# Kernel optimization log

Measured on AMD Instinct MI355X. Metric: run time of the kernel, lower is better.

The kernel has to match this reference:

```python
import jax, jax.numpy as jnp
import numpy as np

B, H, S, D = 4, 16, 2048, 64

def setup_inputs() -> dict:
    key = jax.random.key(0)
    kq, kk, kv = jax.random.split(key, 3)
    return {
        "input_query": jax.random.normal(kq, (B, H, S, D), dtype=jnp.float32),
        "input_key": jax.random.normal(kk, (B, H, S, D), dtype=jnp.float32),
        "input_value": jax.random.normal(kv, (B, H, S, D), dtype=jnp.float32),
    }

def reference(input_query, input_key, input_value):
    # Unscaled, unmasked attention: softmax(Q K^T) V
    scores = jnp.einsum("bhsd,bhtd->bhst", input_query, input_key)  # [B,H,S,S]
    probs = jax.nn.softmax(scores, axis=-1)
    return jnp.einsum("bhst,bhtd->bhsd", probs, input_value)  # [B,H,S,D]
```

## Files before the change

kernel.cpp:

```cpp
#include <hip/hip_runtime.h>
#include <hip/hip_bf16.h>
#include <stdint.h>

#define SEQ 2048
#define DIM 64
#define NH  64
#define KT  32
#define NT  (SEQ / KT)
#define RAW_BYTES  16384
#define FRAG_BYTES 12288
#define KF_BYTES   8192

typedef __attribute__((ext_vector_type(8)))  short    bf16x8;
typedef __attribute__((ext_vector_type(8)))  _Float16 f16x8;
typedef __attribute__((ext_vector_type(16))) float    f32x16;
typedef unsigned int u32;

#if __has_builtin(__builtin_amdgcn_exp2f)
#define EXP2(x) __builtin_amdgcn_exp2f(x)
#else
#define EXP2(x) exp2f(x)
#endif

__device__ __forceinline__ int phi(int s) {
    int h = (s >> 2) & 1, b = s >> 3, i = s & 3;
    return 8 * h + 4 * b + i + (b >= 2 ? 8 : 0);
}
__device__ __forceinline__ short f2bf(float f) {
    union { float f; u32 u; } v; v.f = f;
    u32 r = v.u + 0x7fffu + ((v.u >> 16) & 1u);
    return (short)(r >> 16);
}

__device__ __forceinline__ void stage_tile(const float* gK, const float* gV,
                                           char* raw, int wave, int lane) {
    #pragma unroll
    for (int i = 0; i < 2; ++i) {
        const int P  = wave * 128 + i * 64 + lane;
        const int sk = (P & ~15) | ((P & 15) ^ ((P >> 4) & 7));
        char* dK = raw + (size_t)(wave * 128 + i * 64) * 16;
        char* dV = raw + 8192 + (size_t)(wave * 128 + i * 64) * 16;
        __builtin_amdgcn_global_load_lds(
            (const __attribute__((address_space(1))) u32*)((const char*)gK + (size_t)sk * 16),
            (__attribute__((address_space(3))) u32*)dK, 16, 0, 0);
        __builtin_amdgcn_global_load_lds(
            (const __attribute__((address_space(1))) u32*)((const char*)gV + (size_t)P * 16),
            (__attribute__((address_space(3))) u32*)dV, 16, 0, 0);
    }
}

__device__ __forceinline__ void convert_tile(const char* raw, char* frag, int t) {
    const int lane = t & 63, col = lane & 31, h = lane >> 5;
    {
        const int c = t >> 6;
        const int r = phi(col);
        const int kk = 4 * c + 2 * h;
        const float4* rk = (const float4*)raw;
        float4 a = rk[r * 16 + ((kk    ) ^ (r & 7))];
        float4 b = rk[r * 16 + ((kk + 1) ^ (r & 7))];
        float x[8] = {a.x, a.y, a.z, a.w, b.x, b.y, b.z, b.w};
        f16x8 hi, lo;
        #pragma unroll
        for (int j = 0; j < 8; ++j) {
            _Float16 xh = (_Float16)x[j];
            hi[j] = xh;
            lo[j] = (_Float16)(x[j] - (float)xh);
        }
        *(f16x8*)(frag + (c * 2 + 0) * 1024 + lane * 16) = hi;
        *(f16x8*)(frag + (c * 2 + 1) * 1024 + lane * 16) = lo;
    }
    {
        const int f = t >> 7, c = (t >> 6) & 1;
        const float* rv = (const float*)(raw + 8192);
        bf16x8 v;
        #pragma unroll
        for (int j = 0; j < 8; ++j) {
            int key = phi(16 * c + 8 * h + j);
            v[j] = f2bf(rv[key * 64 + f * 32 + col]);
        }
        *(bf16x8*)(frag + KF_BYTES + (f * 2 + c) * 1024 + lane * 16) = v;
    }
}

__global__ __launch_bounds__(256, 2) void attn_fused(
    const float* __restrict__ Q, const float* __restrict__ K,
    const float* __restrict__ V, float* __restrict__ O)
{
    __shared__ __align__(16) char raw[2][RAW_BYTES];
    __shared__ __align__(16) char frag[2][FRAG_BYTES];

    const int tid  = threadIdx.x;
    const int wave = tid >> 6, lane = tid & 63;
    const int h = lane >> 5, col = lane & 31;
    const int head = blockIdx.x >> 3;
    const int qb = (blockIdx.x & 7) * 256 + wave * 64;
    const size_t base = (size_t)head * SEQ * DIM;
    const float* Kh = K + base;
    const float* Vh = V + base;

    f16x8 qf[2][4];
    #pragma unroll
    for (int qt = 0; qt < 2; ++qt) {
        const float* qr = Q + base + (size_t)(qb + qt * 32 + col) * DIM;
        #pragma unroll
        for (int c = 0; c < 4; ++c)
            #pragma unroll
            for (int j = 0; j < 8; ++j)
                qf[qt][c][j] = (_Float16)(qr[c * 16 + 8 * h + j] * 1.44269504088896f);
    }

    f32x16 z16;
    #pragma unroll
    for (int r = 0; r < 16; ++r) z16[r] = 0.f;
    f32x16 of[2][2];
    of[0][0] = z16; of[0][1] = z16; of[1][0] = z16; of[1][1] = z16;
    float l_own[2] = {0.f, 0.f};

    stage_tile(Kh, Vh, raw[0], wave, lane);
    __syncthreads();
    convert_tile(raw[0], frag[0], tid);
    stage_tile(Kh + KT * DIM, Vh + KT * DIM, raw[1], wave, lane);

    for (int kt = 0; kt < NT; ++kt) {
        __syncthreads();
        if (kt < NT - 2)
            stage_tile(Kh + (size_t)(kt + 2) * KT * DIM,
                       Vh + (size_t)(kt + 2) * KT * DIM, raw[kt & 1], wave, lane);
        const char* cur = frag[kt & 1];

        f32x16 s[2]; s[0] = z16; s[1] = z16;
        #pragma unroll
        for (int c = 0; c < 4; ++c) {
            f16x8 kh = *(const f16x8*)(cur + (c * 2 + 0) * 1024 + lane * 16);
            f16x8 kl = *(const f16x8*)(cur + (c * 2 + 1) * 1024 + lane * 16);
            s[0] = __builtin_amdgcn_mfma_f32_32x32x16_f16(kh, qf[0][c], s[0], 0, 0, 0);
            s[0] = __builtin_amdgcn_mfma_f32_32x32x16_f16(kl, qf[0][c], s[0], 0, 0, 0);
            s[1] = __builtin_amdgcn_mfma_f32_32x32x16_f16(kh, qf[1][c], s[1], 0, 0, 0);
            s[1] = __builtin_amdgcn_mfma_f32_32x32x16_f16(kl, qf[1][c], s[1], 0, 0, 0);
        }

        bf16x8 pfrag[2][2];
        #pragma unroll
        for (int qt = 0; qt < 2; ++qt) {
            float p[16], ls = 0.f;
            #pragma unroll
            for (int r = 0; r < 16; ++r) { p[r] = EXP2(s[qt][r]); ls += p[r]; }
            l_own[qt] += ls;
            u32 pk[8], sw[8];
            #pragma unroll
            for (int m = 0; m < 8; ++m) {
                __hip_bfloat162 b2 = __float22bfloat162_rn(make_float2(p[2 * m], p[2 * m + 1]));
                __builtin_memcpy(&pk[m], &b2, 4);
            }
            #pragma unroll
            for (int m = 0; m < 8; ++m) sw[m] = __shfl_xor(pk[m], 32);
            #pragma unroll
            for (int c = 0; c < 2; ++c) {
                union { u32 w[4]; bf16x8 v; } fr;
                fr.w[0] = h ? sw[4 * c + 2] : pk[4 * c + 0];
                fr.w[1] = h ? sw[4 * c + 3] : pk[4 * c + 1];
                fr.w[2] = h ? pk[4 * c + 2] : sw[4 * c + 0];
                fr.w[3] = h ? pk[4 * c + 3] : sw[4 * c + 1];
                pfrag[qt][c] = fr.v;
            }
        }

        #pragma unroll
        for (int f = 0; f < 2; ++f)
            #pragma unroll
            for (int c = 0; c < 2; ++c) {
                bf16x8 vf = *(const bf16x8*)(cur + KF_BYTES + (f * 2 + c) * 1024 + lane * 16);
                of[0][f] = __builtin_amdgcn_mfma_f32_32x32x16_bf16(pfrag[0][c], vf, of[0][f], 0, 0, 0);
                of[1][f] = __builtin_amdgcn_mfma_f32_32x32x16_bf16(pfrag[1][c], vf, of[1][f], 0, 0, 0);
            }

        if (kt < NT - 1)
            convert_tile(raw[(kt + 1) & 1], frag[(kt + 1) & 1], tid);
    }

    float* op = O + base;
    #pragma unroll
    for (int qt = 0; qt < 2; ++qt) {
        float lall = l_own[qt] + __shfl_xor(l_own[qt], 32);
        float inv = 1.0f / lall;
        #pragma unroll
        for (int r = 0; r < 16; ++r) {
            int qrow = (r & 3) + 8 * (r >> 2) + 4 * h;
            float iq = __shfl(inv, qrow);
            op[(size_t)(qb + qt * 32 + qrow) * DIM + col]      = of[qt][0][r] * iq;
            op[(size_t)(qb + qt * 32 + qrow) * DIM + 32 + col] = of[qt][1][r] * iq;
        }
    }
}

extern "C" void kernel_launch(void* const* d_in, const int* in_sizes, int n_in,
                              void* d_out, int out_size, void* d_ws, size_t ws_size,
                              hipStream_t stream) {
    const float* Q = (const float*)d_in[0];
    const float* K = (const float*)d_in[1];
    const float* V = (const float*)d_in[2];
    float* Out = (float*)d_out;
    (void)d_ws; (void)ws_size;

    attn_fused<<<dim3(NH * (SEQ / 256)), dim3(256), 0, stream>>>(Q, K, V, Out);
}
```

Measured before the change: 238.5 us.

## Load K/V tiles directly into registers, drop raw LDS staging, raise occupancy

Replaces the global_load_lds staging into a raw LDS buffer with direct per-thread global loads into registers, issued one tile ahead and converted into the fragment buffer after compute. This removes 32KB of raw LDS per block, so launch bounds go from 2 to 3 blocks per SM. Block-to-head mapping is also remapped so that consecutive blocks cover different heads. The trade-offs are higher register pressure, a prefetch distance of one tile instead of two, and V loads that gather strided scalars.

```diff
diff --git a/kernel.cpp b/kernel.cpp
--- a/kernel.cpp
+++ b/kernel.cpp
@@ -7,7 +7,6 @@
 #define NH  64
 #define KT  32
 #define NT  (SEQ / KT)
-#define RAW_BYTES  16384
 #define FRAG_BYTES 12288
 #define KF_BYTES   8192
 
@@ -32,33 +31,39 @@
     return (short)(r >> 16);
 }
 
-__device__ __forceinline__ void stage_tile(const float* gK, const float* gV,
-                                           char* raw, int wave, int lane) {
+__global__ __launch_bounds__(256, 3) void attn_fused(
+    const float* __restrict__ Q, const float* __restrict__ K,
+    const float* __restrict__ V, float* __restrict__ O)
+{
+    __shared__ __align__(16) char frag[2][FRAG_BYTES];
+
+    const int tid  = threadIdx.x;
+    const int wave = tid >> 6, lane = tid & 63;
+    const int h = lane >> 5, col = lane & 31;
+
+    const int bid  = blockIdx.x;
+    const int head = (bid & 7) * 8 + ((bid >> 3) & 7);
+    const int qb   = (bid >> 6) * 256 + wave * 64;
+    const size_t base = (size_t)head * SEQ * DIM;
+
+    const float* kbase = K + base + (size_t)phi(col) * DIM + wave * 16 + 8 * h;
+    const int fv = tid >> 7, cv = (tid >> 6) & 1;
+    int vrow[8];
     #pragma unroll
-    for (int i = 0; i < 2; ++i) {
-        const int P  = wave * 128 + i * 64 + lane;
-        const int sk = (P & ~15) | ((P & 15) ^ ((P >> 4) & 7));
-        char* dK = raw + (size_t)(wave * 128 + i * 64) * 16;
-        char* dV = raw + 8192 + (size_t)(wave * 128 + i * 64) * 16;
-        __builtin_amdgcn_global_load_lds(
-            (const __attribute__((address_space(1))) u32*)((const char*)gK + (size_t)sk * 16),
-            (__attribute__((address_space(3))) u32*)dK, 16, 0, 0);
-        __builtin_amdgcn_global_load_lds(
-            (const __attribute__((address_space(1))) u32*)((const char*)gV + (size_t)P * 16),
-            (__attribute__((address_space(3))) u32*)dV, 16, 0, 0);
-    }
-}
+    for (int j = 0; j < 8; ++j) vrow[j] = phi(16 * cv + 8 * h + j);
+    const float* vbase = V + base + fv * 32 + col;
 
-__device__ __forceinline__ void convert_tile(const char* raw, char* frag, int t) {
-    const int lane = t & 63, col = lane & 31, h = lane >> 5;
-    {
-        const int c = t >> 6;
-        const int r = phi(col);
-        const int kk = 4 * c + 2 * h;
-        const float4* rk = (const float4*)raw;
-        float4 a = rk[r * 16 + ((kk    ) ^ (r & 7))];
-        float4 b = rk[r * 16 + ((kk + 1) ^ (r & 7))];
-        float x[8] = {a.x, a.y, a.z, a.w, b.x, b.y, b.z, b.w};
+    float4 ka, kb; float vv[8];
+    auto load_stage = [&](int kt) {
+        const float* kp = kbase + (size_t)kt * (KT * DIM);
+        ka = *(const float4*)(kp);
+        kb = *(const float4*)(kp + 4);
+        const float* vp = vbase + (size_t)kt * (KT * DIM);
+        #pragma unroll
+        for (int j = 0; j < 8; ++j) vv[j] = vp[vrow[j] * DIM];
+    };
+    auto convert = [&](char* dst) {
+        float x[8] = {ka.x, ka.y, ka.z, ka.w, kb.x, kb.y, kb.z, kb.w};
         f16x8 hi, lo;
         #pragma unroll
         for (int j = 0; j < 8; ++j) {
@@ -66,37 +71,13 @@
             hi[j] = xh;
             lo[j] = (_Float16)(x[j] - (float)xh);
         }
-        *(f16x8*)(frag + (c * 2 + 0) * 1024 + lane * 16) = hi;
-        *(f16x8*)(frag + (c * 2 + 1) * 1024 + lane * 16) = lo;
-    }
-    {
-        const int f = t >> 7, c = (t >> 6) & 1;
-        const float* rv = (const float*)(raw + 8192);
+        *(f16x8*)(dst + (wave * 2 + 0) * 1024 + lane * 16) = hi;
+        *(f16x8*)(dst + (wave * 2 + 1) * 1024 + lane * 16) = lo;
         bf16x8 v;
         #pragma unroll
-        for (int j = 0; j < 8; ++j) {
-            int key = phi(16 * c + 8 * h + j);
-            v[j] = f2bf(rv[key * 64 + f * 32 + col]);
-        }
-        *(bf16x8*)(frag + KF_BYTES + (f * 2 + c) * 1024 + lane * 16) = v;
-    }
-}
-
-__global__ __launch_bounds__(256, 2) void attn_fused(
-    const float* __restrict__ Q, const float* __restrict__ K,
-    const float* __restrict__ V, float* __restrict__ O)
-{
-    __shared__ __align__(16) char raw[2][RAW_BYTES];
-    __shared__ __align__(16) char frag[2][FRAG_BYTES];
-
-    const int tid  = threadIdx.x;
-    const int wave = tid >> 6, lane = tid & 63;
-    const int h = lane >> 5, col = lane & 31;
-    const int head = blockIdx.x >> 3;
-    const int qb = (blockIdx.x & 7) * 256 + wave * 64;
-    const size_t base = (size_t)head * SEQ * DIM;
-    const float* Kh = K + base;
-    const float* Vh = V + base;
+        for (int j = 0; j < 8; ++j) v[j] = f2bf(vv[j]);
+        *(bf16x8*)(dst + KF_BYTES + (fv * 2 + cv) * 1024 + lane * 16) = v;
+    };
 
     f16x8 qf[2][4];
     #pragma unroll
@@ -116,16 +97,13 @@
     of[0][0] = z16; of[0][1] = z16; of[1][0] = z16; of[1][1] = z16;
     float l_own[2] = {0.f, 0.f};
 
-    stage_tile(Kh, Vh, raw[0], wave, lane);
-    __syncthreads();
-    convert_tile(raw[0], frag[0], tid);
-    stage_tile(Kh + KT * DIM, Vh + KT * DIM, raw[1], wave, lane);
+    load_stage(0);
+    convert(frag[0]);
 
     for (int kt = 0; kt < NT; ++kt) {
         __syncthreads();
-        if (kt < NT - 2)
-            stage_tile(Kh + (size_t)(kt + 2) * KT * DIM,
-                       Vh + (size_t)(kt + 2) * KT * DIM, raw[kt & 1], wave, lane);
+        if (kt + 1 < NT)
+            load_stage(kt + 1);
         const char* cur = frag[kt & 1];
 
         f32x16 s[2]; s[0] = z16; s[1] = z16;
@@ -174,8 +152,8 @@
                 of[1][f] = __builtin_amdgcn_mfma_f32_32x32x16_bf16(pfrag[1][c], vf, of[1][f], 0, 0, 0);
             }
 
-        if (kt < NT - 1)
-            convert_tile(raw[(kt + 1) & 1], frag[(kt + 1) & 1], tid);
+        if (kt + 1 < NT)
+            convert(frag[(kt + 1) & 1]);
     }
 
     float* op = O + base;
```

New measurement: 382.1 us. 1.6x slower.

## Triple-buffer raw K/V staging with fine-grained waitcnt barriers and head-interleaved block mapping

Applied to the files above, without the earlier changes.

Grows the raw LDS staging buffer from two to three slots, so the async global-to-LDS load for tile kt+2 can be issued before the current tile is converted without reusing a slot that is still being read. The full __syncthreads is replaced by explicit vmcnt/lgkmcnt waits plus s_barrier, letting up to one tile's loads stay in flight across the barrier. MFMA sections are wrapped in s_setprio, and the block-to-head mapping is permuted so consecutive blocks work on different heads. This adds LDS usage (about 16KB more per block), which may reduce occupancy, and the hand-counted vmcnt values rely on a fixed number of loads per stage.

```diff
diff --git a/kernel.cpp b/kernel.cpp
--- a/kernel.cpp
+++ b/kernel.cpp
@@ -86,14 +86,16 @@
     const float* __restrict__ Q, const float* __restrict__ K,
     const float* __restrict__ V, float* __restrict__ O)
 {
-    __shared__ __align__(16) char raw[2][RAW_BYTES];
+    __shared__ __align__(16) char raw[3][RAW_BYTES];
     __shared__ __align__(16) char frag[2][FRAG_BYTES];
 
     const int tid  = threadIdx.x;
     const int wave = tid >> 6, lane = tid & 63;
     const int h = lane >> 5, col = lane & 31;
-    const int head = blockIdx.x >> 3;
-    const int qb = (blockIdx.x & 7) * 256 + wave * 64;
+
+    const int bid  = blockIdx.x;
+    const int head = (bid & 7) * 8 + ((bid >> 3) & 7);
+    const int qb   = (bid >> 6) * 256 + wave * 64;
     const size_t base = (size_t)head * SEQ * DIM;
     const float* Kh = K + base;
     const float* Vh = V + base;
@@ -117,18 +119,27 @@
     float l_own[2] = {0.f, 0.f};
 
     stage_tile(Kh, Vh, raw[0], wave, lane);
-    __syncthreads();
+    stage_tile(Kh + KT * DIM, Vh + KT * DIM, raw[1], wave, lane);
+    asm volatile("s_waitcnt vmcnt(4)" ::: "memory");
+    __builtin_amdgcn_s_barrier();
+    __builtin_amdgcn_sched_barrier(0);
     convert_tile(raw[0], frag[0], tid);
-    stage_tile(Kh + KT * DIM, Vh + KT * DIM, raw[1], wave, lane);
+
+    int stg_i = 2;
+    int cvt_i = 1;
 
     for (int kt = 0; kt < NT; ++kt) {
-        __syncthreads();
-        if (kt < NT - 2)
+        asm volatile("s_waitcnt lgkmcnt(0)" ::: "memory");
+        __builtin_amdgcn_s_barrier();
+        __builtin_amdgcn_sched_barrier(0);
+
+        if (kt + 2 < NT)
             stage_tile(Kh + (size_t)(kt + 2) * KT * DIM,
-                       Vh + (size_t)(kt + 2) * KT * DIM, raw[kt & 1], wave, lane);
+                       Vh + (size_t)(kt + 2) * KT * DIM, raw[stg_i], wave, lane);
         const char* cur = frag[kt & 1];
 
         f32x16 s[2]; s[0] = z16; s[1] = z16;
+        __builtin_amdgcn_s_setprio(1);
         #pragma unroll
         for (int c = 0; c < 4; ++c) {
             f16x8 kh = *(const f16x8*)(cur + (c * 2 + 0) * 1024 + lane * 16);
@@ -138,6 +149,7 @@
             s[1] = __builtin_amdgcn_mfma_f32_32x32x16_f16(kh, qf[1][c], s[1], 0, 0, 0);
             s[1] = __builtin_amdgcn_mfma_f32_32x32x16_f16(kl, qf[1][c], s[1], 0, 0, 0);
         }
+        __builtin_amdgcn_s_setprio(0);
 
         bf16x8 pfrag[2][2];
         #pragma unroll
@@ -165,6 +177,7 @@
             }
         }
 
+        __builtin_amdgcn_s_setprio(1);
         #pragma unroll
         for (int f = 0; f < 2; ++f)
             #pragma unroll
@@ -173,9 +186,17 @@
                 of[0][f] = __builtin_amdgcn_mfma_f32_32x32x16_bf16(pfrag[0][c], vf, of[0][f], 0, 0, 0);
                 of[1][f] = __builtin_amdgcn_mfma_f32_32x32x16_bf16(pfrag[1][c], vf, of[1][f], 0, 0, 0);
             }
-
-        if (kt < NT - 1)
-            convert_tile(raw[(kt + 1) & 1], frag[(kt + 1) & 1], tid);
+        __builtin_amdgcn_s_setprio(0);
+
+        if (kt + 1 < NT) {
+            if (kt + 2 < NT) asm volatile("s_waitcnt vmcnt(4)" ::: "memory");
+            else             asm volatile("s_waitcnt vmcnt(0)" ::: "memory");
+            __builtin_amdgcn_s_barrier();
+            __builtin_amdgcn_sched_barrier(0);
+            convert_tile(raw[cvt_i], frag[(kt + 1) & 1], tid);
+        }
+        stg_i = (stg_i == 2) ? 0 : stg_i + 1;
+        cvt_i = (cvt_i == 2) ? 0 : cvt_i + 1;
     }
 
     float* op = O + base;
```

New measurement: 244.5 us. +2.5%, slower.
